# Optimization experiments

Hardware: AMD Instinct MI355X
Metric: run time of the kernel (lower is better)

## Reference

```python
import jax, jax.numpy as jnp
import numpy as np

VOCAB = 50257
CUTOFF = (10000, 50000, 50257)  # cutoff + [vocab_size] per __init__
D = 1024
B, T = 2, 1024
HEAD_SZ = CUTOFF[0] + 2  # cutoff[0] + n_tail_clusters


def setup_inputs() -> dict:
    key = jax.random.key(0)
    ks = jax.random.split(key, 7)
    def xavier(k, shp):
        # xavier_uniform as in init_weights
        bound = np.sqrt(6.0 / (shp[0] + shp[1])).astype(np.float32)
        return jax.random.uniform(k, shp, dtype=jnp.float32, minval=-bound, maxval=bound)
    return {
        "input": jax.random.normal(ks[0], (B, T, D), dtype=jnp.float32),
        "target": jax.random.randint(ks[1], (B, T), 0, VOCAB),
        "head_w": xavier(ks[2], (HEAD_SZ, D)),              # [10002, 1024]
        "t0_a": xavier(ks[3], (D, D)),                       # [1024, 1024]
        "t0_b": xavier(ks[4], (CUTOFF[1] - CUTOFF[0], D)),   # [40000, 1024]
        "t1_a": xavier(ks[5], (D // 4, D)),                  # [256, 1024]
        "t1_b": xavier(ks[6], (CUTOFF[2] - CUTOFF[1], D // 4)),  # [207, 256]
    }


def reference(input, target, head_w, t0_a, t0_b, t1_a, t1_b):
    # Faithful jax version of AdaptiveSoftmax.get_log_prob (eval mode, dropout=0).
    # Torch updates log_probs[idxs, start:end] only for rows whose target lies in
    # cluster i (leaving other rows zero); we express the same gather->small GEMM
    # chain->log_softmax->prior-add->scatter via masked writes (jit-friendly).
    bsz, length, dim = input.shape
    xi = input.reshape(-1, dim)                     # [N, D]
    tgt = target.reshape(-1)                        # [N]

    head_lp = jax.nn.log_softmax(xi @ head_w.T, axis=1)        # [N, HEAD_SZ]
    tail_priors = head_lp[:, CUTOFF[0] - 1:HEAD_SZ - 1]        # [N, 2]

    log_probs = jnp.zeros((xi.shape[0], VOCAB), dtype=input.dtype)
    log_probs = log_probs.at[:, :HEAD_SZ].set(head_lp)

    tails = ((t0_a, t0_b), (t1_a, t1_b))
    for i, (wa, wb) in enumerate(tails):
        lo, hi = CUTOFF[i], CUTOFF[i + 1]
        mask = (tgt >= lo) & (tgt < hi)                        # [N]
        # Linear(D, D//4**i) -> Linear(D//4**i, hi-lo), then log_softmax + prior
        tail_lp = jax.nn.log_softmax((xi @ wa.T) @ wb.T, axis=1) + tail_priors[:, i:i + 1]
        log_probs = log_probs.at[:, lo:hi].set(
            jnp.where(mask[:, None], tail_lp, log_probs[:, lo:hi]))
    return log_probs.reshape(bsz, length, VOCAB)
```

## Files before the change

### kernel.cpp

```cpp
#include <hip/hip_runtime.h>

typedef unsigned short u16;
typedef unsigned int u32;
typedef __attribute__((ext_vector_type(4))) float f32x4;
typedef __bf16 bf16x8 __attribute__((ext_vector_type(8)));
typedef __attribute__((ext_vector_type(8))) unsigned short u16x8;

__device__ __forceinline__ u16 f2bf(float x) {
    u32 u = __builtin_bit_cast(u32, x);
    u += 0x7FFFu + ((u >> 16) & 1u);
    return (u16)(u >> 16);
}
__device__ __forceinline__ float bf2f(u16 u) {
    return __builtin_bit_cast(float, ((u32)u) << 16);
}
__device__ __forceinline__ void gld_lds16(void* lds, const void* g) {
    __builtin_amdgcn_global_load_lds(
        (const __attribute__((address_space(1))) void*)g,
        (__attribute__((address_space(3))) void*)lds, 16, 0, 0);
}

__device__ __forceinline__ size_t pack_base_tail(long row) {
    return (size_t)row * 100514 + 59936 - ((row * 2) & 7);
}
__device__ __forceinline__ size_t pack_base_head(long row) {
    return (size_t)row * 100514 + 20480 - ((row * 2) & 7);
}

__global__ __launch_bounds__(256) void cvt_all(const float* __restrict__ x,
                                               const float* __restrict__ hw,
                                               const float* __restrict__ t0a,
                                               const float* __restrict__ t1a,
                                               const float* __restrict__ t0b,
                                               const float* __restrict__ t1b,
                                               u16* __restrict__ XI, u16* __restrict__ HW,
                                               u16* __restrict__ TAB, u16* __restrict__ T0B,
                                               u16* __restrict__ T1B) {
    int b = blockIdx.x;
    const float* src; u16* dst; int n, b0, nb;
    if (b < 80)        { src = x;    dst = XI;            n = 2097152;  b0 = 0;    nb = 80;   }
    else if (b < 472)  { src = hw;   dst = HW;            n = 10242048; b0 = 80;   nb = 392;  }
    else if (b < 512)  { src = t0a;  dst = TAB;           n = 1048576;  b0 = 472;  nb = 40;   }
    else if (b < 522)  { src = t1a;  dst = TAB + 1048576; n = 262144;   b0 = 512;  nb = 10;   }
    else if (b < 2086) { src = t0b;  dst = T0B;           n = 40960000; b0 = 522;  nb = 1564; }
    else if (b < 2090) { src = t1b;  dst = T1B;           n = 65792;    b0 = 2086; nb = 4;    }
    else if (b < 2100) { src = 0;    dst = HW + 10242048; n = 243712;   b0 = 2090; nb = 10;   }
    else               { src = 0;    dst = T0B + 40960000; n = 196608;  b0 = 2100; nb = 8;    }
    int i0 = (b - b0) * 1024 + threadIdx.x * 4;
    int stride = nb * 1024;
    if (src) {
        for (int i = i0; i < n; i += stride) {
            float4 v = *(const float4*)(src + i);
            ushort4 o;
            o.x = f2bf(v.x); o.y = f2bf(v.y); o.z = f2bf(v.z); o.w = f2bf(v.w);
            *(ushort4*)(dst + i) = o;
        }
    } else {
        ushort4 z = {0, 0, 0, 0};
        for (int i = i0; i < n; i += stride) *(ushort4*)(dst + i) = z;
    }
}

__global__ __launch_bounds__(256) void build_map(const int* __restrict__ tgt,
                                                 int* __restrict__ rowlist,
                                                 int* __restrict__ cntbuf) {
    __shared__ int cs[257];
    int t = threadIdx.x;
    int cnt_local = 0;
    int mk[8];
#pragma unroll
    for (int k = 0; k < 8; k++) {
        int tg = tgt[t * 8 + k];
        mk[k] = (tg >= 10000 && tg < 50000) ? 1 : 0;
        cnt_local += mk[k];
    }
    cs[t + 1] = cnt_local;
    __syncthreads();
    if (t == 0) {
        cs[0] = 0;
        for (int i = 1; i <= 256; i++) cs[i] += cs[i - 1];
        cntbuf[0] = cs[256];
        cntbuf[1] = (cs[256] + 255) & ~255;
    }
    __syncthreads();
    int cnt = cs[256];
    int offm = cs[t];
    int offu = cnt + (t * 8 - cs[t]);
#pragma unroll
    for (int k = 0; k < 8; k++) {
        if (mk[k]) rowlist[offm++] = t * 8 + k;
        else       rowlist[offu++] = t * 8 + k;
    }
}

template <int TAIL>
__global__ __launch_bounds__(512, 1) void gemm256p(const u16* __restrict__ A,
                                                   const u16* __restrict__ B,
                                                   u16* __restrict__ outpk,
                                                   const int* __restrict__ rowlist,
                                                   const int* __restrict__ cntbuf,
                                                   float* __restrict__ part) {
    const int NY = TAIL ? 157 : 40;
    const int l = blockIdx.y * 8 + blockIdx.x;
    const int w = (l & 7) * NY + (l >> 3);
    const int m0 = (w & 7) * 256, n0 = (w >> 3) * 256;
    if (TAIL) { if (m0 >= cntbuf[1]) return; }
    __shared__ u16 lds[65536];
    const int tid = threadIdx.x;
    const int lane = tid & 63, wv = tid >> 6;
    const int wm = wv >> 2, wn = wv & 3;
    const int lr = lane & 15, hi = lane >> 4;

    const int rp = ((tid >> 7) << 4) + (tid & 15);
    const int kp = ((tid >> 4) & 7) * 8;
    const u16 *pA[2][2], *pB[2][2];
#pragma unroll
    for (int h = 0; h < 2; h++) {
#pragma unroll
        for (int c = 0; c < 2; c++) {
            int row = h * 128 + rp + c * 64;
            if (TAIL) pA[h][c] = A + (size_t)rowlist[m0 + row] * 1280 + kp;
            else      pA[h][c] = A + (size_t)(m0 + row) * 1024 + kp;
            pB[h][c] = B + (size_t)(n0 + row) * 1024 + kp;
        }
    }

    f32x4 acc[8][4] = {};
    bf16x8 Bf[4][2], Af[2][2];

    auto stA = [&](int s, int h, int t) {
        u16* d = lds + s * 16384 + h * 8192 + tid * 8;
        int ko = t * 64;
        gld_lds16(d, pA[h][0] + ko);
        gld_lds16(d + 4096, pA[h][1] + ko);
    };
    auto stB = [&](int s, int h, int t) {
        u16* d = lds + 32768 + s * 16384 + h * 8192 + tid * 8;
        int ko = t * 64;
        gld_lds16(d, pB[h][0] + ko);
        gld_lds16(d + 4096, pB[h][1] + ko);
    };
    auto rdB = [&](int s) {
        const u16* base = lds + 32768 + s * 16384 + (wn >> 1) * 8192 + (wn & 1) * 4096 + hi * 128 + lr * 8;
#pragma unroll
        for (int j = 0; j < 4; j++)
#pragma unroll
            for (int ks = 0; ks < 2; ks++)
                Bf[j][ks] = *(const bf16x8*)(base + j * 1024 + ks * 512);
    };
    auto rdA = [&](int s, int p) {
        const u16* base = lds + s * 16384 + wm * 8192 + p * 2048 + hi * 128 + lr * 8;
#pragma unroll
        for (int m = 0; m < 2; m++)
#pragma unroll
            for (int ks = 0; ks < 2; ks++)
                Af[m][ks] = *(const bf16x8*)(base + m * 1024 + ks * 512);
    };
    auto mf = [&](int p) {
        __builtin_amdgcn_s_setprio(1);
#pragma unroll
        for (int m = 0; m < 2; m++)
#pragma unroll
            for (int j = 0; j < 4; j++)
#pragma unroll
                for (int ks = 0; ks < 2; ks++)
                    acc[p * 2 + m][j] = __builtin_amdgcn_mfma_f32_16x16x32_bf16(
                        Af[m][ks], Bf[j][ks], acc[p * 2 + m][j], 0, 0, 0);
        __builtin_amdgcn_s_setprio(0);
    };

#define BAR_()   __builtin_amdgcn_s_barrier()
#define LGKM0_() do { asm volatile("s_waitcnt lgkmcnt(0)" ::: "memory"); \
                      __builtin_amdgcn_sched_barrier(0); } while (0)
#define VM4_()   asm volatile("s_waitcnt vmcnt(4)" ::: "memory")
#define VM0_()   asm volatile("s_waitcnt vmcnt(0)" ::: "memory")

    stA(0, 0, 0); stA(0, 1, 0); stB(0, 0, 0); stB(0, 1, 0);
    VM0_();
    stB(1, 0, 1); stB(1, 1, 1);
    BAR_();

    auto iter = [&](int t0, bool full) {
        rdB(0); rdA(0, 0);
        stA(1, 0, t0 + 1);
        BAR_(); LGKM0_(); mf(0); BAR_();
        rdA(0, 1);
        stA(1, 1, t0 + 1);
        __builtin_amdgcn_sched_barrier(0);
        if (full) stB(0, 0, t0 + 2);
        BAR_(); LGKM0_(); mf(1); BAR_();
        rdA(0, 2);
        if (full) stB(0, 1, t0 + 2);
        BAR_(); LGKM0_(); mf(2); BAR_();
        rdA(0, 3);
        if (full) { VM4_(); } else { VM0_(); }
        BAR_(); LGKM0_(); mf(3); BAR_();
        rdB(1); rdA(1, 0);
        if (full) stA(0, 0, t0 + 2);
        BAR_(); LGKM0_(); mf(0); BAR_();
        rdA(1, 1);
        if (full) { stA(0, 1, t0 + 2);
                    __builtin_amdgcn_sched_barrier(0);
                    stB(1, 0, t0 + 3); }
        BAR_(); LGKM0_(); mf(1); BAR_();
        rdA(1, 2);
        if (full) stB(1, 1, t0 + 3);
        BAR_(); LGKM0_(); mf(2); BAR_();
        rdA(1, 3);
        if (full) VM4_();
        BAR_(); LGKM0_(); mf(3); BAR_();
    };
#pragma unroll 1
    for (int i = 0; i < 7; i++) iter(2 * i, true);
    iter(14, false);

#undef BAR_
#undef LGKM0_
#undef VM4_
#undef VM0_

    const int cr = hi * 4, cc = lr;
    const int climit = TAIL ? 40000 : 10002;
    const int pstride = TAIL ? 628 : 160;
#pragma unroll
    for (int m = 0; m < 8; m++) {
#pragma unroll
        for (int q = 0; q < 4; q++) {
            int r = m0 + wm * 128 + m * 16 + cr + q;
            long orow = TAIL ? rowlist[r] : r;
            size_t base = TAIL ? pack_base_tail(orow) : pack_base_head(orow);
            u16* dst = outpk + base + n0 + wn * 64 + cc;
            float s = 0.f;
#pragma unroll
            for (int j = 0; j < 4; j++) {
                float v = acc[m][j][q];
                dst[j * 16] = f2bf(v);
                int col = n0 + wn * 64 + j * 16 + cc;
                s += (col < climit) ? __expf(v) : 0.f;
            }
            s += __shfl_xor(s, 1); s += __shfl_xor(s, 2);
            s += __shfl_xor(s, 4); s += __shfl_xor(s, 8);
            if (cc == 0) part[(size_t)r * pstride + (n0 >> 6) + wn] = s;
        }
    }
}

__global__ __launch_bounds__(256) void gemm_nt_bf16(const u16* __restrict__ A, int lda,
                                                    const u16* __restrict__ B, int ldb,
                                                    u16* __restrict__ Cb, long ldc, int K) {
    __shared__ u16 lA[128 * 32];
    __shared__ u16 lB[128 * 32];
    const int tid = threadIdx.x;
    const int lane = tid & 63, wv = tid >> 6;
    const int m0 = blockIdx.x * 128, n0 = blockIdx.y * 128;

    const u16* gA0 = A + (size_t)(m0 + (tid >> 2)) * lda + (tid & 3) * 8;
    const u16* gB0 = B + (size_t)(n0 + (tid >> 2)) * ldb + (tid & 3) * 8;
    char* dA = (char*)lA + wv * 1024;
    char* dB = (char*)lB + wv * 1024;

    f32x4 acc[4][4] = {};
    const int wm = wv >> 1, wn = wv & 1;
    const int lr = lane & 15;
    const int lk = (lane >> 4) * 8;

    for (int kt = 0; kt < K; kt += 32) {
        __syncthreads();
        gld_lds16(dA, gA0);
        gld_lds16(dA + 4096, gA0 + 64 * (size_t)lda);
        gld_lds16(dB, gB0);
        gld_lds16(dB + 4096, gB0 + 64 * (size_t)ldb);
        gA0 += 32; gB0 += 32;
        __syncthreads();

        bf16x8 af[4], bfr[4];
#pragma unroll
        for (int i = 0; i < 4; i++) {
            af[i]  = *(const bf16x8*)(lA + (wm * 64 + i * 16 + lr) * 32 + lk);
            bfr[i] = *(const bf16x8*)(lB + (wn * 64 + i * 16 + lr) * 32 + lk);
        }
#pragma unroll
        for (int i = 0; i < 4; i++)
#pragma unroll
            for (int j = 0; j < 4; j++)
                acc[i][j] = __builtin_amdgcn_mfma_f32_16x16x32_bf16(af[i], bfr[j], acc[i][j], 0, 0, 0);
    }

    const int cr = (lane >> 4) * 4;
    const int cc = lane & 15;
#pragma unroll
    for (int i = 0; i < 4; i++) {
        int rbase = m0 + wm * 64 + i * 16 + cr;
#pragma unroll
        for (int j = 0; j < 4; j++) {
            int c = n0 + wn * 64 + j * 16 + cc;
#pragma unroll
            for (int q = 0; q < 4; q++)
                Cb[(size_t)(rbase + q) * (size_t)ldc + c] = f2bf(acc[i][j][q]);
        }
    }
}

__global__ __launch_bounds__(256) void head_norm(float* __restrict__ out,
                                                 float* __restrict__ stats,
                                                 const float* __restrict__ parth) {
    const int row = blockIdx.x, tid = threadIdx.x;
    float s = (tid < 160) ? parth[(size_t)row * 160 + tid] : 0.f;
#pragma unroll
    for (int o = 32; o; o >>= 1) s += __shfl_xor(s, o);
    __shared__ float red[4];
    if ((tid & 63) == 0) red[tid >> 6] = s;
    __syncthreads();
    float logZ = __logf(red[0] + red[1] + red[2] + red[3]);
    const u16* pk = (const u16*)out + pack_base_head(row);
    float* p = out + (size_t)row * 50257;
    for (int k = 0; k < 5; k++) {
        int c0 = k * 2048 + tid * 8;
        if (c0 + 8 <= 10002) {
            u16x8 xv = *(const u16x8*)(pk + c0);
#pragma unroll
            for (int z = 0; z < 8; z++) p[c0 + z] = bf2f(xv[z]) - logZ;
        } else if (c0 < 10002) {
            for (int z = 0; c0 + z < 10002; z++) p[c0 + z] = bf2f(pk[c0 + z]) - logZ;
        }
    }
    if (tid == 0) {
        float* st = stats + row * 8;
        float l0 = bf2f(pk[9999]) - logZ;
        float l1 = bf2f(pk[10000]) - logZ;
        float l2 = bf2f(pk[10001]) - logZ;
        st[0] = l0; st[1] = l1; st[2] = l1; st[3] = l2;
    }
}

__global__ __launch_bounds__(256) void tail0_norm(float* __restrict__ out,
                                                  const int* __restrict__ rowlist,
                                                  const int* __restrict__ cntbuf,
                                                  const float* __restrict__ ST,
                                                  const float* __restrict__ PART) {
    const int b = blockIdx.x, tid = threadIdx.x;
    const int cnt = cntbuf[0];
    const long row = rowlist[b];
    float* p = out + (size_t)row * 50257 + 10000;
    __shared__ float red[4];
    if (b < cnt) {
        float s = 0.f;
        for (int c = tid; c < 628; c += 256) s += PART[(size_t)b * 628 + c];
#pragma unroll
        for (int o = 32; o; o >>= 1) s += __shfl_xor(s, o);
        if ((tid & 63) == 0) red[tid >> 6] = s;
        __syncthreads();
        float Aa = __logf(red[0] + red[1] + red[2] + red[3]) - ST[row * 8 + 0];
        const u16* src = (const u16*)out + pack_base_tail(row);
        for (int k = 0; k < 5; k++) {
            float v[4][8];
#pragma unroll
            for (int g = 0; g < 4; g++) {
                int o = 2048 * g + tid * 8;
                if (o < 8000) {
                    u16x8 xv = *(const u16x8*)(src + 8000 * k + o);
#pragma unroll
                    for (int z = 0; z < 8; z++) v[g][z] = bf2f(xv[z]);
                }
            }
            __syncthreads();
#pragma unroll
            for (int g = 0; g < 4; g++) {
                int o = 2048 * g + tid * 8;
                if (o < 8000) {
                    int e = 8000 * k + o;
#pragma unroll
                    for (int z = 0; z < 8; z++) p[e + z] = v[g][z] - Aa;
                }
            }
            __syncthreads();
        }
    } else {
        float v0 = ST[row * 8 + 2], v1 = ST[row * 8 + 3];
        for (int e = tid; e < 40000; e += 256) p[e] = 0.f;
        if (tid == 0) { p[0] = v0; p[1] = v1; }
    }
}

__global__ __launch_bounds__(256) void tail1_kernel(float* __restrict__ out,
                                                    const int* __restrict__ tgt,
                                                    const u16* __restrict__ proj,
                                                    const u16* __restrict__ t1b,
                                                    const float* __restrict__ stats) {
    const int row = blockIdx.x, tid = threadIdx.x;
    float* p = out + (size_t)row * 50257 + 50000;
    int t = tgt[row];
    if (t < 50000) {
        for (int c = tid; c < 257; c += 256) p[c] = 0.f;
        return;
    }
    __shared__ float pr[256];
    __shared__ float lg[257];
    __shared__ float red[4];
    pr[tid] = bf2f(proj[(size_t)row * 1280 + 1024 + tid]);
    __syncthreads();
    for (int c = tid; c < 257; c += 256) {
        const u16* w = t1b + c * 256;
        float acc = 0.f;
        for (int k = 0; k < 256; k++) acc += bf2f(w[k]) * pr[k];
        lg[c] = acc;
    }
    __syncthreads();
    float s = 0.f;
    for (int c = tid; c < 257; c += 256) s += __expf(lg[c]);
#pragma unroll
    for (int o = 32; o; o >>= 1) s += __shfl_xor(s, o);
    if ((tid & 63) == 0) red[tid >> 6] = s;
    __syncthreads();
    float A = __logf(red[0] + red[1] + red[2] + red[3]) - stats[row * 8 + 1];
    for (int c = tid; c < 257; c += 256) p[c] = lg[c] - A;
}

#define OFF_XI    0UL
#define OFF_HEADW 4194304UL
#define OFF_TAB   25165824UL
#define OFF_T0B   27787264UL
#define OFF_T1B   110100480UL
#define OFF_PROJ  110232064UL
#define OFF_ST    115474944UL
#define OFF_PART  115540480UL
#define OFF_PARTH 120685056UL
#define OFF_MAP   121995776UL
#define OFF_CNT   122003968UL

extern "C" void kernel_launch(void* const* d_in, const int* in_sizes, int n_in,
                              void* d_out, int out_size, void* d_ws, size_t ws_size,
                              hipStream_t stream) {
    const float* x   = (const float*)d_in[0];
    const int*   tgt = (const int*)d_in[1];
    const float* hw  = (const float*)d_in[2];
    const float* t0a = (const float*)d_in[3];
    const float* t0b = (const float*)d_in[4];
    const float* t1a = (const float*)d_in[5];
    const float* t1b = (const float*)d_in[6];
    float* out = (float*)d_out;
    char* ws = (char*)d_ws;

    u16* XI     = (u16*)(ws + OFF_XI);
    u16* HW     = (u16*)(ws + OFF_HEADW);
    u16* TAB    = (u16*)(ws + OFF_TAB);
    u16* T0B    = (u16*)(ws + OFF_T0B);
    u16* T1B    = (u16*)(ws + OFF_T1B);
    u16* PROJ   = (u16*)(ws + OFF_PROJ);
    float* ST   = (float*)(ws + OFF_ST);
    float* PART = (float*)(ws + OFF_PART);
    float* PARTH = (float*)(ws + OFF_PARTH);
    int* MAP    = (int*)(ws + OFF_MAP);
    int* CNT    = (int*)(ws + OFF_CNT);

    cvt_all<<<2108, 256, 0, stream>>>(x, hw, t0a, t1a, t0b, t1b, XI, HW, TAB, T0B, T1B);

    build_map<<<1, 256, 0, stream>>>(tgt, MAP, CNT);

    gemm256p<0><<<dim3(8, 40), 512, 0, stream>>>(XI, HW, (u16*)d_out, nullptr, nullptr, PARTH);

    head_norm<<<2048, 256, 0, stream>>>(out, ST, PARTH);

    gemm_nt_bf16<<<dim3(16, 10), 256, 0, stream>>>(XI, 1024, TAB, 1024, PROJ, 1280L, 1024);

    gemm256p<1><<<dim3(8, 157), 512, 0, stream>>>(PROJ, T0B, (u16*)d_out, MAP, CNT, PART);

    tail0_norm<<<2048, 256, 0, stream>>>(out, MAP, CNT, ST, PART);

    tail1_kernel<<<2048, 256, 0, stream>>>(out, tgt, PROJ, T1B, ST);
}
```

Before: 567.1 us.

## Merge eight launches into four fused kernels covering conversion, projection, GEMMs and normalisation

Folds build_map into the first conversion kernel, runs the projection GEMM alongside the large t0b conversion in one launch, merges the head and tail GEMMs into a single grid, and combines head_norm, tail0_norm and tail1 into one per-row kernel that keeps priors in registers instead of a stats buffer. The aim is to cut launch overhead and the serialisation gaps between small kernels, and to let independent work share the machine. In exchange, blocks in a merged grid now differ in how much work they do, and the fused norm kernel issues extra barriers per row.

```diff
diff --git a/kernel.cpp b/kernel.cpp
--- a/kernel.cpp
+++ b/kernel.cpp
@@ -27,26 +27,10 @@
     return (size_t)row * 100514 + 20480 - ((row * 2) & 7);
 }
 
-__global__ __launch_bounds__(256) void cvt_all(const float* __restrict__ x,
-                                               const float* __restrict__ hw,
-                                               const float* __restrict__ t0a,
-                                               const float* __restrict__ t1a,
-                                               const float* __restrict__ t0b,
-                                               const float* __restrict__ t1b,
-                                               u16* __restrict__ XI, u16* __restrict__ HW,
-                                               u16* __restrict__ TAB, u16* __restrict__ T0B,
-                                               u16* __restrict__ T1B) {
-    int b = blockIdx.x;
-    const float* src; u16* dst; int n, b0, nb;
-    if (b < 80)        { src = x;    dst = XI;            n = 2097152;  b0 = 0;    nb = 80;   }
-    else if (b < 472)  { src = hw;   dst = HW;            n = 10242048; b0 = 80;   nb = 392;  }
-    else if (b < 512)  { src = t0a;  dst = TAB;           n = 1048576;  b0 = 472;  nb = 40;   }
-    else if (b < 522)  { src = t1a;  dst = TAB + 1048576; n = 262144;   b0 = 512;  nb = 10;   }
-    else if (b < 2086) { src = t0b;  dst = T0B;           n = 40960000; b0 = 522;  nb = 1564; }
-    else if (b < 2090) { src = t1b;  dst = T1B;           n = 65792;    b0 = 2086; nb = 4;    }
-    else if (b < 2100) { src = 0;    dst = HW + 10242048; n = 243712;   b0 = 2090; nb = 10;   }
-    else               { src = 0;    dst = T0B + 40960000; n = 196608;  b0 = 2100; nb = 8;    }
-    int i0 = (b - b0) * 1024 + threadIdx.x * 4;
+__device__ __forceinline__ void cvt_range(const float* __restrict__ src,
+                                          u16* __restrict__ dst, int n,
+                                          int bloc, int nb) {
+    int i0 = bloc * 1024 + threadIdx.x * 4;
     int stride = nb * 1024;
     if (src) {
         for (int i = i0; i < n; i += stride) {
@@ -61,9 +45,22 @@
     }
 }
 
-__global__ __launch_bounds__(256) void build_map(const int* __restrict__ tgt,
-                                                 int* __restrict__ rowlist,
-                                                 int* __restrict__ cntbuf) {
+__global__ __launch_bounds__(256) void cvt1(const float* __restrict__ x,
+                                            const float* __restrict__ hw,
+                                            const float* __restrict__ t0a,
+                                            const float* __restrict__ t1a,
+                                            const float* __restrict__ t1b,
+                                            const int* __restrict__ tgt,
+                                            u16* __restrict__ XI, u16* __restrict__ HW,
+                                            u16* __restrict__ TAB, u16* __restrict__ T1B,
+                                            int* __restrict__ rowlist, int* __restrict__ cntbuf) {
+    int b = blockIdx.x;
+    if (b < 80)       { cvt_range(x,   XI,            2097152,  b,       80);  return; }
+    if (b < 472)      { cvt_range(hw,  HW,            10242048, b - 80,  392); return; }
+    if (b < 512)      { cvt_range(t0a, TAB,           1048576,  b - 472, 40);  return; }
+    if (b < 522)      { cvt_range(t1a, TAB + 1048576, 262144,   b - 512, 10);  return; }
+    if (b < 526)      { cvt_range(t1b, T1B,           65792,    b - 522, 4);   return; }
+    if (b < 536)      { cvt_range(0,   HW + 10242048, 243712,   b - 526, 10);  return; }
     __shared__ int cs[257];
     int t = threadIdx.x;
     int cnt_local = 0;
@@ -93,18 +90,87 @@
     }
 }
 
-template <int TAIL>
-__global__ __launch_bounds__(512, 1) void gemm256p(const u16* __restrict__ A,
-                                                   const u16* __restrict__ B,
+__global__ __launch_bounds__(256) void proj_cvt(const u16* __restrict__ A,
+                                                const u16* __restrict__ B,
+                                                u16* __restrict__ Cb,
+                                                const float* __restrict__ t0b,
+                                                u16* __restrict__ T0B) {
+    int b = blockIdx.x;
+    if (b >= 160) {
+        if (b < 1724) cvt_range(t0b, T0B, 40960000, b - 160, 1564);
+        else          cvt_range(0, T0B + 40960000, 196608, b - 1724, 8);
+        return;
+    }
+    __shared__ u16 lA[128 * 32];
+    __shared__ u16 lB[128 * 32];
+    const int tid = threadIdx.x;
+    const int lane = tid & 63, wv = tid >> 6;
+    const int m0 = (b & 15) * 128, n0 = (b >> 4) * 128;
+
+    const u16* gA0 = A + (size_t)(m0 + (tid >> 2)) * 1024 + (tid & 3) * 8;
+    const u16* gB0 = B + (size_t)(n0 + (tid >> 2)) * 1024 + (tid & 3) * 8;
+    char* dA = (char*)lA + wv * 1024;
+    char* dB = (char*)lB + wv * 1024;
+
+    f32x4 acc[4][4] = {};
+    const int wm = wv >> 1, wn = wv & 1;
+    const int lr = lane & 15;
+    const int lk = (lane >> 4) * 8;
+
+    for (int kt = 0; kt < 1024; kt += 32) {
+        __syncthreads();
+        gld_lds16(dA, gA0);
+        gld_lds16(dA + 4096, gA0 + 64 * 1024);
+        gld_lds16(dB, gB0);
+        gld_lds16(dB + 4096, gB0 + 64 * 1024);
+        gA0 += 32; gB0 += 32;
+        __syncthreads();
+
+        bf16x8 af[4], bfr[4];
+#pragma unroll
+        for (int i = 0; i < 4; i++) {
+            af[i]  = *(const bf16x8*)(lA + (wm * 64 + i * 16 + lr) * 32 + lk);
+            bfr[i] = *(const bf16x8*)(lB + (wn * 64 + i * 16 + lr) * 32 + lk);
+        }
+#pragma unroll
+        for (int i = 0; i < 4; i++)
+#pragma unroll
+            for (int j = 0; j < 4; j++)
+                acc[i][j] = __builtin_amdgcn_mfma_f32_16x16x32_bf16(af[i], bfr[j], acc[i][j], 0, 0, 0);
+    }
+
+    const int cr = (lane >> 4) * 4;
+    const int cc = lane & 15;
+#pragma unroll
+    for (int i = 0; i < 4; i++) {
+        int rbase = m0 + wm * 64 + i * 16 + cr;
+#pragma unroll
+        for (int j = 0; j < 4; j++) {
+            int c = n0 + wn * 64 + j * 16 + cc;
+#pragma unroll
+            for (int q = 0; q < 4; q++)
+                Cb[(size_t)(rbase + q) * 1280 + c] = f2bf(acc[i][j][q]);
+        }
+    }
+}
+
+__global__ __launch_bounds__(512, 1) void gemm_all(const u16* __restrict__ XI,
+                                                   const u16* __restrict__ PROJ,
+                                                   const u16* __restrict__ HW,
+                                                   const u16* __restrict__ T0B,
                                                    u16* __restrict__ outpk,
                                                    const int* __restrict__ rowlist,
                                                    const int* __restrict__ cntbuf,
+                                                   float* __restrict__ parth,
                                                    float* __restrict__ part) {
-    const int NY = TAIL ? 157 : 40;
-    const int l = blockIdx.y * 8 + blockIdx.x;
+    const bool tail = blockIdx.y >= 40;
+    const int NY = tail ? 157 : 40;
+    const int l = (blockIdx.y - (tail ? 40 : 0)) * 8 + blockIdx.x;
     const int w = (l & 7) * NY + (l >> 3);
     const int m0 = (w & 7) * 256, n0 = (w >> 3) * 256;
-    if (TAIL) { if (m0 >= cntbuf[1]) return; }
+    if (tail && m0 >= cntbuf[1]) return;
+    const u16* A = tail ? PROJ : XI;
+    const u16* B = tail ? T0B : HW;
     __shared__ u16 lds[65536];
     const int tid = threadIdx.x;
     const int lane = tid & 63, wv = tid >> 6;
@@ -119,7 +185,7 @@
 #pragma unroll
         for (int c = 0; c < 2; c++) {
             int row = h * 128 + rp + c * 64;
-            if (TAIL) pA[h][c] = A + (size_t)rowlist[m0 + row] * 1280 + kp;
+            if (tail) pA[h][c] = A + (size_t)rowlist[m0 + row] * 1280 + kp;
             else      pA[h][c] = A + (size_t)(m0 + row) * 1024 + kp;
             pB[h][c] = B + (size_t)(n0 + row) * 1024 + kp;
         }
@@ -220,15 +286,16 @@
 #undef VM0_
 
     const int cr = hi * 4, cc = lr;
-    const int climit = TAIL ? 40000 : 10002;
-    const int pstride = TAIL ? 628 : 160;
+    const int climit = tail ? 40000 : 10002;
+    const int pstride = tail ? 628 : 160;
+    float* pbuf = tail ? part : parth;
 #pragma unroll
     for (int m = 0; m < 8; m++) {
 #pragma unroll
         for (int q = 0; q < 4; q++) {
             int r = m0 + wm * 128 + m * 16 + cr + q;
-            long orow = TAIL ? rowlist[r] : r;
-            size_t base = TAIL ? pack_base_tail(orow) : pack_base_head(orow);
+            long orow = tail ? rowlist[r] : r;
+            size_t base = tail ? pack_base_tail(orow) : pack_base_head(orow);
             u16* dst = outpk + base + n0 + wn * 64 + cc;
             float s = 0.f;
 #pragma unroll
@@ -240,117 +307,58 @@
             }
             s += __shfl_xor(s, 1); s += __shfl_xor(s, 2);
             s += __shfl_xor(s, 4); s += __shfl_xor(s, 8);
-            if (cc == 0) part[(size_t)r * pstride + (n0 >> 6) + wn] = s;
-        }
-    }
-}
-
-__global__ __launch_bounds__(256) void gemm_nt_bf16(const u16* __restrict__ A, int lda,
-                                                    const u16* __restrict__ B, int ldb,
-                                                    u16* __restrict__ Cb, long ldc, int K) {
-    __shared__ u16 lA[128 * 32];
-    __shared__ u16 lB[128 * 32];
-    const int tid = threadIdx.x;
-    const int lane = tid & 63, wv = tid >> 6;
-    const int m0 = blockIdx.x * 128, n0 = blockIdx.y * 128;
-
-    const u16* gA0 = A + (size_t)(m0 + (tid >> 2)) * lda + (tid & 3) * 8;
-    const u16* gB0 = B + (size_t)(n0 + (tid >> 2)) * ldb + (tid & 3) * 8;
-    char* dA = (char*)lA + wv * 1024;
-    char* dB = (char*)lB + wv * 1024;
-
-    f32x4 acc[4][4] = {};
-    const int wm = wv >> 1, wn = wv & 1;
-    const int lr = lane & 15;
-    const int lk = (lane >> 4) * 8;
-
-    for (int kt = 0; kt < K; kt += 32) {
-        __syncthreads();
-        gld_lds16(dA, gA0);
-        gld_lds16(dA + 4096, gA0 + 64 * (size_t)lda);
-        gld_lds16(dB, gB0);
-        gld_lds16(dB + 4096, gB0 + 64 * (size_t)ldb);
-        gA0 += 32; gB0 += 32;
-        __syncthreads();
-
-        bf16x8 af[4], bfr[4];
-#pragma unroll
-        for (int i = 0; i < 4; i++) {
-            af[i]  = *(const bf16x8*)(lA + (wm * 64 + i * 16 + lr) * 32 + lk);
-            bfr[i] = *(const bf16x8*)(lB + (wn * 64 + i * 16 + lr) * 32 + lk);
-        }
-#pragma unroll
-        for (int i = 0; i < 4; i++)
-#pragma unroll
-            for (int j = 0; j < 4; j++)
-                acc[i][j] = __builtin_amdgcn_mfma_f32_16x16x32_bf16(af[i], bfr[j], acc[i][j], 0, 0, 0);
-    }
-
-    const int cr = (lane >> 4) * 4;
-    const int cc = lane & 15;
-#pragma unroll
-    for (int i = 0; i < 4; i++) {
-        int rbase = m0 + wm * 64 + i * 16 + cr;
-#pragma unroll
-        for (int j = 0; j < 4; j++) {
-            int c = n0 + wn * 64 + j * 16 + cc;
-#pragma unroll
-            for (int q = 0; q < 4; q++)
-                Cb[(size_t)(rbase + q) * (size_t)ldc + c] = f2bf(acc[i][j][q]);
-        }
-    }
-}
-
-__global__ __launch_bounds__(256) void head_norm(float* __restrict__ out,
-                                                 float* __restrict__ stats,
-                                                 const float* __restrict__ parth) {
-    const int row = blockIdx.x, tid = threadIdx.x;
-    float s = (tid < 160) ? parth[(size_t)row * 160 + tid] : 0.f;
+            if (cc == 0) pbuf[(size_t)r * pstride + (n0 >> 6) + wn] = s;
+        }
+    }
+}
+
+__global__ __launch_bounds__(256) void norm_all(float* __restrict__ out,
+                                                const int* __restrict__ tgt,
+                                                const int* __restrict__ rowlist,
+                                                const int* __restrict__ cntbuf,
+                                                const float* __restrict__ PARTH,
+                                                const float* __restrict__ PART,
+                                                const u16* __restrict__ proj,
+                                                const u16* __restrict__ t1b) {
+    const int b = blockIdx.x, tid = threadIdx.x;
+    const int cnt = cntbuf[0];
+    const long row = rowlist[b];
+    __shared__ float red[4];
+    __shared__ float pr[256];
+    __shared__ float lg[257];
+    float* p0 = out + (size_t)row * 50257;
+
+    float s = (tid < 160) ? PARTH[(size_t)row * 160 + tid] : 0.f;
 #pragma unroll
     for (int o = 32; o; o >>= 1) s += __shfl_xor(s, o);
-    __shared__ float red[4];
     if ((tid & 63) == 0) red[tid >> 6] = s;
     __syncthreads();
-    float logZ = __logf(red[0] + red[1] + red[2] + red[3]);
-    const u16* pk = (const u16*)out + pack_base_head(row);
-    float* p = out + (size_t)row * 50257;
+    float logZh = __logf(red[0] + red[1] + red[2] + red[3]);
+    const u16* pkh = (const u16*)out + pack_base_head(row);
+    float prior0 = bf2f(pkh[9999]) - logZh;
+    float l1 = bf2f(pkh[10000]) - logZh;
+    float l2 = bf2f(pkh[10001]) - logZh;
     for (int k = 0; k < 5; k++) {
         int c0 = k * 2048 + tid * 8;
         if (c0 + 8 <= 10002) {
-            u16x8 xv = *(const u16x8*)(pk + c0);
-#pragma unroll
-            for (int z = 0; z < 8; z++) p[c0 + z] = bf2f(xv[z]) - logZ;
+            u16x8 xv = *(const u16x8*)(pkh + c0);
+#pragma unroll
+            for (int z = 0; z < 8; z++) p0[c0 + z] = bf2f(xv[z]) - logZh;
         } else if (c0 < 10002) {
-            for (int z = 0; c0 + z < 10002; z++) p[c0 + z] = bf2f(pk[c0 + z]) - logZ;
-        }
-    }
-    if (tid == 0) {
-        float* st = stats + row * 8;
-        float l0 = bf2f(pk[9999]) - logZ;
-        float l1 = bf2f(pk[10000]) - logZ;
-        float l2 = bf2f(pk[10001]) - logZ;
-        st[0] = l0; st[1] = l1; st[2] = l1; st[3] = l2;
-    }
-}
-
-__global__ __launch_bounds__(256) void tail0_norm(float* __restrict__ out,
-                                                  const int* __restrict__ rowlist,
-                                                  const int* __restrict__ cntbuf,
-                                                  const float* __restrict__ ST,
-                                                  const float* __restrict__ PART) {
-    const int b = blockIdx.x, tid = threadIdx.x;
-    const int cnt = cntbuf[0];
-    const long row = rowlist[b];
-    float* p = out + (size_t)row * 50257 + 10000;
-    __shared__ float red[4];
+            for (int z = 0; c0 + z < 10002; z++) p0[c0 + z] = bf2f(pkh[c0 + z]) - logZh;
+        }
+    }
+    __syncthreads();
+
+    float* p = p0 + 10000;
     if (b < cnt) {
-        float s = 0.f;
-        for (int c = tid; c < 628; c += 256) s += PART[(size_t)b * 628 + c];
-#pragma unroll
-        for (int o = 32; o; o >>= 1) s += __shfl_xor(s, o);
-        if ((tid & 63) == 0) red[tid >> 6] = s;
+        float s2 = 0.f;
+        for (int c = tid; c < 628; c += 256) s2 += PART[(size_t)b * 628 + c];
+#pragma unroll
+        for (int o = 32; o; o >>= 1) s2 += __shfl_xor(s2, o);
+        if ((tid & 63) == 0) red[tid >> 6] = s2;
         __syncthreads();
-        float Aa = __logf(red[0] + red[1] + red[2] + red[3]) - ST[row * 8 + 0];
+        float Aa = __logf(red[0] + red[1] + red[2] + red[3]) - prior0;
         const u16* src = (const u16*)out + pack_base_tail(row);
         for (int k = 0; k < 5; k++) {
             float v[4][8];
@@ -376,44 +384,34 @@
             __syncthreads();
         }
     } else {
-        float v0 = ST[row * 8 + 2], v1 = ST[row * 8 + 3];
         for (int e = tid; e < 40000; e += 256) p[e] = 0.f;
-        if (tid == 0) { p[0] = v0; p[1] = v1; }
-    }
-}
-
-__global__ __launch_bounds__(256) void tail1_kernel(float* __restrict__ out,
-                                                    const int* __restrict__ tgt,
-                                                    const u16* __restrict__ proj,
-                                                    const u16* __restrict__ t1b,
-                                                    const float* __restrict__ stats) {
-    const int row = blockIdx.x, tid = threadIdx.x;
-    float* p = out + (size_t)row * 50257 + 50000;
+        if (tid == 0) { p[0] = l1; p[1] = l2; }
+        __syncthreads();
+    }
+
+    float* p5 = p0 + 50000;
     int t = tgt[row];
     if (t < 50000) {
-        for (int c = tid; c < 257; c += 256) p[c] = 0.f;
+        for (int c = tid; c < 257; c += 256) p5[c] = 0.f;
         return;
     }
-    __shared__ float pr[256];
-    __shared__ float lg[257];
-    __shared__ float red[4];
     pr[tid] = bf2f(proj[(size_t)row * 1280 + 1024 + tid]);
     __syncthreads();
     for (int c = tid; c < 257; c += 256) {
-        const u16* w = t1b + c * 256;
+        const u16* wp = t1b + c * 256;
         float acc = 0.f;
-        for (int k = 0; k < 256; k++) acc += bf2f(w[k]) * pr[k];
+        for (int k = 0; k < 256; k++) acc += bf2f(wp[k]) * pr[k];
         lg[c] = acc;
     }
     __syncthreads();
-    float s = 0.f;
-    for (int c = tid; c < 257; c += 256) s += __expf(lg[c]);
-#pragma unroll
-    for (int o = 32; o; o >>= 1) s += __shfl_xor(s, o);
-    if ((tid & 63) == 0) red[tid >> 6] = s;
-    __syncthreads();
-    float A = __logf(red[0] + red[1] + red[2] + red[3]) - stats[row * 8 + 1];
-    for (int c = tid; c < 257; c += 256) p[c] = lg[c] - A;
+    float s1 = 0.f;
+    for (int c = tid; c < 257; c += 256) s1 += __expf(lg[c]);
+#pragma unroll
+    for (int o = 32; o; o >>= 1) s1 += __shfl_xor(s1, o);
+    if ((tid & 63) == 0) red[tid >> 6] = s1;
+    __syncthreads();
+    float A = __logf(red[0] + red[1] + red[2] + red[3]) - l1;
+    for (int c = tid; c < 257; c += 256) p5[c] = lg[c] - A;
 }
 
 #define OFF_XI    0UL
@@ -422,11 +420,10 @@
 #define OFF_T0B   27787264UL
 #define OFF_T1B   110100480UL
 #define OFF_PROJ  110232064UL
-#define OFF_ST    115474944UL
-#define OFF_PART  115540480UL
-#define OFF_PARTH 120685056UL
-#define OFF_MAP   121995776UL
-#define OFF_CNT   122003968UL
+#define OFF_PART  115474944UL
+#define OFF_PARTH 120619520UL
+#define OFF_MAP   121930240UL
+#define OFF_CNT   121938432UL
 
 extern "C" void kernel_launch(void* const* d_in, const int* in_sizes, int n_in,
                               void* d_out, int out_size, void* d_ws, size_t ws_size,
@@ -447,25 +444,16 @@
     u16* T0B    = (u16*)(ws + OFF_T0B);
     u16* T1B    = (u16*)(ws + OFF_T1B);
     u16* PROJ   = (u16*)(ws + OFF_PROJ);
-    float* ST   = (float*)(ws + OFF_ST);
     float* PART = (float*)(ws + OFF_PART);
     float* PARTH = (float*)(ws + OFF_PARTH);
     int* MAP    = (int*)(ws + OFF_MAP);
     int* CNT    = (int*)(ws + OFF_CNT);
 
-    cvt_all<<<2108, 256, 0, stream>>>(x, hw, t0a, t1a, t0b, t1b, XI, HW, TAB, T0B, T1B);
-
-    build_map<<<1, 256, 0, stream>>>(tgt, MAP, CNT);
-
-    gemm256p<0><<<dim3(8, 40), 512, 0, stream>>>(XI, HW, (u16*)d_out, nullptr, nullptr, PARTH);
-
-    head_norm<<<2048, 256, 0, stream>>>(out, ST, PARTH);
-
-    gemm_nt_bf16<<<dim3(16, 10), 256, 0, stream>>>(XI, 1024, TAB, 1024, PROJ, 1280L, 1024);
-
-    gemm256p<1><<<dim3(8, 157), 512, 0, stream>>>(PROJ, T0B, (u16*)d_out, MAP, CNT, PART);
-
-    tail0_norm<<<2048, 256, 0, stream>>>(out, MAP, CNT, ST, PART);
-
-    tail1_kernel<<<2048, 256, 0, stream>>>(out, tgt, PROJ, T1B, ST);
-}
+    cvt1<<<537, 256, 0, stream>>>(x, hw, t0a, t1a, t1b, tgt, XI, HW, TAB, T1B, MAP, CNT);
+
+    proj_cvt<<<1732, 256, 0, stream>>>(XI, TAB, PROJ, t0b, T0B);
+
+    gemm_all<<<dim3(8, 197), 512, 0, stream>>>(XI, PROJ, HW, T0B, (u16*)d_out, MAP, CNT, PARTH, PART);
+
+    norm_all<<<2048, 256, 0, stream>>>(out, tgt, MAP, CNT, PARTH, PART, PROJ, T1B);
+}
```

After: 546.2 us. -3.7%, faster.
